# Performance work log

Hardware: AMD Instinct MI355X
Metric: run time of the kernel (lower is better)

The kernel has to match this reference:

```python
import jax, jax.numpy as jnp
import numpy as np
from jax.scipy.linalg import expm

B, T, D = 4096, 256, 64


def setup_inputs() -> dict:
    key = jax.random.key(0)
    k1, k2, k3, k4 = jax.random.split(key, 4)
    X0 = jax.random.normal(k1, (B, D), dtype=jnp.float32)
    t_span = jnp.sort(jax.random.uniform(k2, (T,), dtype=jnp.float32))
    W = jax.random.normal(k3, (D, D), dtype=jnp.float32) * 0.05  # keep exp(A t) well-conditioned
    x_star = jax.random.normal(k4, (D,), dtype=jnp.float32)
    mask = jnp.ones((D, D), dtype=bool)
    return {"X0": X0, "t_span": t_span, "W": W, "x_star": x_star, "mask": mask}


def reference(X0, t_span, W, x_star, mask):
    # A_eff = W * mask  (elementwise sparsity mask on the system matrix)
    A = W * mask.astype(W.dtype)                       # [d, d]
    # E[t] = expm(A * t)  -- batched matrix exponential over T time points
    E = jax.vmap(expm)(A[None, :, :] * t_span[:, None, None])  # [T, d, d]
    # out[b,t,k] = sum_d E[t,k,d] * (X0 - x_star)[b,d] + x_star[k]
    out = jnp.einsum('bd,tkd->btk', X0 - x_star, E) + x_star   # [B, T, d]
    return out
```

## Files before the change

### kernel.cpp

```cpp
#include <hip/hip_runtime.h>

#define DD 64
#define TT 256
#define BB 4096
#define KTERMS 16

__global__ __launch_bounds__(512, 1) void expm_taylor(
    const float* __restrict__ W, const int* __restrict__ mask,
    const float* __restrict__ t_span, float* __restrict__ Eg)
{
    __shared__ float P[DD][DD + 1];
    __shared__ float M[DD][DD];

    const int t   = blockIdx.x;
    const float tv = t_span[t];
    const int tid = threadIdx.x;

    #pragma unroll
    for (int i = 0; i < 8; ++i) {
        const int idx = tid + i * 512;
        const int r = idx >> 6, c = idx & 63;
        const float w = W[idx] * tv;
        P[r][c] = (mask[idx] != 0) ? w : 0.0f;
    }
    __syncthreads();

    #pragma unroll
    for (int i = 0; i < 8; ++i) {
        const int idx = tid + i * 512;
        const int r = idx >> 6, c = idx & 63;
        M[r][c] = P[r][c] * (1.0f / (float)KTERMS) + ((r == c) ? 1.0f : 0.0f);
    }
    __syncthreads();

    const int ct = tid & 15;
    const int rt = tid >> 4;
    const int c0 = ct * 4;
    const int r0 = rt * 2;

    for (int j = KTERMS - 1; j >= 1; --j) {
        const float inv = 1.0f / (float)j;
        float a0[4] = {0.f, 0.f, 0.f, 0.f};
        float a1[4] = {0.f, 0.f, 0.f, 0.f};
        #pragma unroll
        for (int k = 0; k < DD; ++k) {
            const float p0 = P[r0 + 0][k];
            const float p1 = P[r0 + 1][k];
            const float4 b = *reinterpret_cast<const float4*>(&M[k][c0]);
            a0[0] += p0 * b.x; a0[1] += p0 * b.y; a0[2] += p0 * b.z; a0[3] += p0 * b.w;
            a1[0] += p1 * b.x; a1[1] += p1 * b.y; a1[2] += p1 * b.z; a1[3] += p1 * b.w;
        }
        __syncthreads();
        M[r0 + 0][c0 + 0] = a0[0] * inv + ((r0 + 0 == c0 + 0) ? 1.f : 0.f);
        M[r0 + 0][c0 + 1] = a0[1] * inv + ((r0 + 0 == c0 + 1) ? 1.f : 0.f);
        M[r0 + 0][c0 + 2] = a0[2] * inv + ((r0 + 0 == c0 + 2) ? 1.f : 0.f);
        M[r0 + 0][c0 + 3] = a0[3] * inv + ((r0 + 0 == c0 + 3) ? 1.f : 0.f);
        M[r0 + 1][c0 + 0] = a1[0] * inv + ((r0 + 1 == c0 + 0) ? 1.f : 0.f);
        M[r0 + 1][c0 + 1] = a1[1] * inv + ((r0 + 1 == c0 + 1) ? 1.f : 0.f);
        M[r0 + 1][c0 + 2] = a1[2] * inv + ((r0 + 1 == c0 + 2) ? 1.f : 0.f);
        M[r0 + 1][c0 + 3] = a1[3] * inv + ((r0 + 1 == c0 + 3) ? 1.f : 0.f);
        __syncthreads();
    }

    #pragma unroll
    for (int i = 0; i < 8; ++i) {
        const int idx = tid + i * 512;
        const int r = idx >> 6, c = idx & 63;
        Eg[(size_t)t * (DD * DD) + idx] = M[r][c];
    }
}

__global__ __launch_bounds__(256, 1) void propagate(
    const float* __restrict__ X0, const float* __restrict__ xs,
    const float* __restrict__ Eg, float* __restrict__ out)
{
    __shared__ float Ys[64][68];
    __shared__ float Es[64][68];

    const int t   = blockIdx.x;
    const int b0  = blockIdx.y << 6;
    const int tid = threadIdx.x;

    {
        const int f   = tid & 15;
        const int row = tid >> 4;
        const float4 xv = reinterpret_cast<const float4*>(xs)[f];
        #pragma unroll
        for (int p = 0; p < 4; ++p) {
            const int rr = row + p * 16;
            float4 v = reinterpret_cast<const float4*>(X0 + (size_t)(b0 + rr) * DD)[f];
            v.x -= xv.x; v.y -= xv.y; v.z -= xv.z; v.w -= xv.w;
            *reinterpret_cast<float4*>(&Ys[rr][f * 4]) = v;
        }
    }
    {
        const float4* Esrc = reinterpret_cast<const float4*>(Eg + (size_t)t * (DD * DD));
        #pragma unroll
        for (int p = 0; p < 4; ++p) {
            const int ch = tid + p * 256;
            const int k  = ch >> 4;
            const int d0 = (ch & 15) * 4;
            const float4 e = Esrc[ch];
            Es[d0 + 0][k] = e.x;
            Es[d0 + 1][k] = e.y;
            Es[d0 + 2][k] = e.z;
            Es[d0 + 3][k] = e.w;
        }
    }
    __syncthreads();

    const int ct = tid & 15;
    const int bt = tid >> 4;
    const int c0 = ct * 4;
    const int bb = bt * 4;

    float acc[4][4] = {{0.f}};
    #pragma unroll
    for (int d = 0; d < DD; ++d) {
        const float4 e = *reinterpret_cast<const float4*>(&Es[d][c0]);
        #pragma unroll
        for (int i = 0; i < 4; ++i) {
            const float y = Ys[bb + i][d];
            acc[i][0] += y * e.x;
            acc[i][1] += y * e.y;
            acc[i][2] += y * e.z;
            acc[i][3] += y * e.w;
        }
    }

    const float4 xv = reinterpret_cast<const float4*>(xs)[ct];
    #pragma unroll
    for (int i = 0; i < 4; ++i) {
        float4 o;
        o.x = acc[i][0] + xv.x;
        o.y = acc[i][1] + xv.y;
        o.z = acc[i][2] + xv.z;
        o.w = acc[i][3] + xv.w;
        float* dst = out + ((size_t)(b0 + bb + i) * TT + t) * DD + c0;
        *reinterpret_cast<float4*>(dst) = o;
    }
}

extern "C" void kernel_launch(void* const* d_in, const int* in_sizes, int n_in,
                              void* d_out, int out_size, void* d_ws, size_t ws_size,
                              hipStream_t stream)
{
    const float* X0     = (const float*)d_in[0];
    const float* t_span = (const float*)d_in[1];
    const float* W      = (const float*)d_in[2];
    const float* xs     = (const float*)d_in[3];
    const int*   mask   = (const int*)d_in[4];
    float*       out    = (float*)d_out;
    float*       Eg     = (float*)d_ws;

    expm_taylor<<<TT, 512, 0, stream>>>(W, mask, t_span, Eg);
    propagate<<<dim3(TT, BB / 64), 256, 0, stream>>>(X0, xs, Eg, out);
}
```

Baseline: 383.3 us.

## Use split-bf16 MFMA for propagation GEMM with swizzled LDS layout

Replaces the FP32 FMA inner product in the propagate kernel with bf16 MFMA 16x16x32 instructions, splitting each operand into high and low bf16 parts and using three cross-products to approximate fp32 accuracy. Operands are converted on load and stored in XOR-swizzled shared memory to avoid bank conflicts. This aims to cut ALU time in the batched GEMM, but adds conversion work and changes output stores to scalar writes with narrower contiguous segments, plus a small accuracy loss from dropping the low-low term.

Measured after the change: 333.1 us. 13.1% less time.

```diff
diff --git a/kernel.cpp b/kernel.cpp
--- a/kernel.cpp
+++ b/kernel.cpp
@@ -4,6 +4,18 @@
 #define TT 256
 #define BB 4096
 #define KTERMS 16
+
+typedef __attribute__((ext_vector_type(8))) short bf16x8;
+typedef __attribute__((ext_vector_type(4))) float f32x4;
+
+__device__ inline unsigned short f32_to_bf16_rne(float x) {
+    unsigned int u = __float_as_uint(x);
+    unsigned int r = (u + 0x7FFFu + ((u >> 16) & 1u)) >> 16;
+    return (unsigned short)r;
+}
+__device__ inline float bf16_to_f32(unsigned short h) {
+    return __uint_as_float(((unsigned int)h) << 16);
+}
 
 __global__ __launch_bounds__(512, 1) void expm_taylor(
     const float* __restrict__ W, const int* __restrict__ mask,
@@ -70,12 +82,14 @@
     }
 }
 
-__global__ __launch_bounds__(256, 1) void propagate(
+__global__ __launch_bounds__(256, 1) void propagate_mfma(
     const float* __restrict__ X0, const float* __restrict__ xs,
     const float* __restrict__ Eg, float* __restrict__ out)
 {
-    __shared__ float Ys[64][68];
-    __shared__ float Es[64][68];
+    __shared__ __align__(16) unsigned short Yh[DD * DD];
+    __shared__ __align__(16) unsigned short Yl[DD * DD];
+    __shared__ __align__(16) unsigned short Ehs[DD * DD];
+    __shared__ __align__(16) unsigned short Els[DD * DD];
 
     const int t   = blockIdx.x;
     const int b0  = blockIdx.y << 6;
@@ -85,59 +99,80 @@
         const int f   = tid & 15;
         const int row = tid >> 4;
         const float4 xv = reinterpret_cast<const float4*>(xs)[f];
-        #pragma unroll
-        for (int p = 0; p < 4; ++p) {
-            const int rr = row + p * 16;
-            float4 v = reinterpret_cast<const float4*>(X0 + (size_t)(b0 + rr) * DD)[f];
-            v.x -= xv.x; v.y -= xv.y; v.z -= xv.z; v.w -= xv.w;
-            *reinterpret_cast<float4*>(&Ys[rr][f * 4]) = v;
-        }
-    }
-    {
         const float4* Esrc = reinterpret_cast<const float4*>(Eg + (size_t)t * (DD * DD));
         #pragma unroll
         for (int p = 0; p < 4; ++p) {
-            const int ch = tid + p * 256;
-            const int k  = ch >> 4;
-            const int d0 = (ch & 15) * 4;
-            const float4 e = Esrc[ch];
-            Es[d0 + 0][k] = e.x;
-            Es[d0 + 1][k] = e.y;
-            Es[d0 + 2][k] = e.z;
-            Es[d0 + 3][k] = e.w;
+            const int r = row + p * 16;
+            const int byte = r * 128 + f * 8;
+            const int swz  = byte ^ ((r & 7) << 4);
+
+            float4 v = reinterpret_cast<const float4*>(X0 + (size_t)(b0 + r) * DD)[f];
+            v.x -= xv.x; v.y -= xv.y; v.z -= xv.z; v.w -= xv.w;
+            ushort4 h, l;
+            h.x = f32_to_bf16_rne(v.x); l.x = f32_to_bf16_rne(v.x - bf16_to_f32(h.x));
+            h.y = f32_to_bf16_rne(v.y); l.y = f32_to_bf16_rne(v.y - bf16_to_f32(h.y));
+            h.z = f32_to_bf16_rne(v.z); l.z = f32_to_bf16_rne(v.z - bf16_to_f32(h.z));
+            h.w = f32_to_bf16_rne(v.w); l.w = f32_to_bf16_rne(v.w - bf16_to_f32(h.w));
+            *reinterpret_cast<ushort4*>(reinterpret_cast<char*>(Yh) + swz) = h;
+            *reinterpret_cast<ushort4*>(reinterpret_cast<char*>(Yl) + swz) = l;
+
+            const float4 e = Esrc[r * 16 + f];
+            ushort4 eh, el;
+            eh.x = f32_to_bf16_rne(e.x); el.x = f32_to_bf16_rne(e.x - bf16_to_f32(eh.x));
+            eh.y = f32_to_bf16_rne(e.y); el.y = f32_to_bf16_rne(e.y - bf16_to_f32(eh.y));
+            eh.z = f32_to_bf16_rne(e.z); el.z = f32_to_bf16_rne(e.z - bf16_to_f32(eh.z));
+            eh.w = f32_to_bf16_rne(e.w); el.w = f32_to_bf16_rne(e.w - bf16_to_f32(eh.w));
+            *reinterpret_cast<ushort4*>(reinterpret_cast<char*>(Ehs) + swz) = eh;
+            *reinterpret_cast<ushort4*>(reinterpret_cast<char*>(Els) + swz) = el;
         }
     }
     __syncthreads();
 
-    const int ct = tid & 15;
-    const int bt = tid >> 4;
-    const int c0 = ct * 4;
-    const int bb = bt * 4;
+    const int lane = tid & 63;
+    const int wave = tid >> 6;
+    const int g    = lane >> 4;
+    const int r16  = lane & 15;
 
-    float acc[4][4] = {{0.f}};
+    const int arow  = wave * 16 + r16;
+    const int abyte = arow * 128 + g * 16;
+    const int asw0  = abyte ^ ((arow & 7) << 4);
+    const int asw1  = (abyte + 64) ^ ((arow & 7) << 4);
+    const bf16x8 ah0 = *reinterpret_cast<const bf16x8*>(reinterpret_cast<const char*>(Yh) + asw0);
+    const bf16x8 ah1 = *reinterpret_cast<const bf16x8*>(reinterpret_cast<const char*>(Yh) + asw1);
+    const bf16x8 al0 = *reinterpret_cast<const bf16x8*>(reinterpret_cast<const char*>(Yl) + asw0);
+    const bf16x8 al1 = *reinterpret_cast<const bf16x8*>(reinterpret_cast<const char*>(Yl) + asw1);
+
+    f32x4 acc[4];
     #pragma unroll
-    for (int d = 0; d < DD; ++d) {
-        const float4 e = *reinterpret_cast<const float4*>(&Es[d][c0]);
-        #pragma unroll
-        for (int i = 0; i < 4; ++i) {
-            const float y = Ys[bb + i][d];
-            acc[i][0] += y * e.x;
-            acc[i][1] += y * e.y;
-            acc[i][2] += y * e.z;
-            acc[i][3] += y * e.w;
-        }
+    for (int nt = 0; nt < 4; ++nt) acc[nt] = (f32x4){0.f, 0.f, 0.f, 0.f};
+
+    #pragma unroll
+    for (int nt = 0; nt < 4; ++nt) {
+        const int brow  = nt * 16 + r16;
+        const int bbyte = brow * 128 + g * 16;
+        const int bsw0  = bbyte ^ ((brow & 7) << 4);
+        const int bsw1  = (bbyte + 64) ^ ((brow & 7) << 4);
+        const bf16x8 bh0 = *reinterpret_cast<const bf16x8*>(reinterpret_cast<const char*>(Ehs) + bsw0);
+        const bf16x8 bh1 = *reinterpret_cast<const bf16x8*>(reinterpret_cast<const char*>(Ehs) + bsw1);
+        const bf16x8 bl0 = *reinterpret_cast<const bf16x8*>(reinterpret_cast<const char*>(Els) + bsw0);
+        const bf16x8 bl1 = *reinterpret_cast<const bf16x8*>(reinterpret_cast<const char*>(Els) + bsw1);
+
+        acc[nt] = __builtin_amdgcn_mfma_f32_16x16x32_bf16(ah0, bh0, acc[nt], 0, 0, 0);
+        acc[nt] = __builtin_amdgcn_mfma_f32_16x16x32_bf16(ah1, bh1, acc[nt], 0, 0, 0);
+        acc[nt] = __builtin_amdgcn_mfma_f32_16x16x32_bf16(al0, bh0, acc[nt], 0, 0, 0);
+        acc[nt] = __builtin_amdgcn_mfma_f32_16x16x32_bf16(al1, bh1, acc[nt], 0, 0, 0);
+        acc[nt] = __builtin_amdgcn_mfma_f32_16x16x32_bf16(ah0, bl0, acc[nt], 0, 0, 0);
+        acc[nt] = __builtin_amdgcn_mfma_f32_16x16x32_bf16(ah1, bl1, acc[nt], 0, 0, 0);
     }
 
-    const float4 xv = reinterpret_cast<const float4*>(xs)[ct];
     #pragma unroll
-    for (int i = 0; i < 4; ++i) {
-        float4 o;
-        o.x = acc[i][0] + xv.x;
-        o.y = acc[i][1] + xv.y;
-        o.z = acc[i][2] + xv.z;
-        o.w = acc[i][3] + xv.w;
-        float* dst = out + ((size_t)(b0 + bb + i) * TT + t) * DD + c0;
-        *reinterpret_cast<float4*>(dst) = o;
+    for (int nt = 0; nt < 4; ++nt) {
+        const float xsv = xs[nt * 16 + r16];
+        #pragma unroll
+        for (int r = 0; r < 4; ++r) {
+            const int m = wave * 16 + g * 4 + r;
+            out[((size_t)(b0 + m) * TT + t) * DD + nt * 16 + r16] = acc[nt][r] + xsv;
+        }
     }
 }
 
@@ -154,5 +189,5 @@
     float*       Eg     = (float*)d_ws;
 
     expm_taylor<<<TT, 512, 0, stream>>>(W, mask, t_span, Eg);
-    propagate<<<dim3(TT, BB / 64), 256, 0, stream>>>(X0, xs, Eg, out);
+    propagate_mfma<<<dim3(TT, BB / 64), 256, 0, stream>>>(X0, xs, Eg, out);
 }
```
